# Kernel optimization log

Measured on AMD Instinct MI355X. Metric: run time of the kernel, lower is better.

## Reference

```python
import jax, jax.numpy as jnp
import numpy as np

N = 4096          # detections per frame
M = 8192          # memory entries (tracks + backdrops)
D = 256           # embed_dim (hardcoded in module)
NUM_CLASSES = 80
OBJ_THR = 0.3
INIT_THR = 0.7
MATCH_THR = 0.5
NMS_CONF_THR = 0.5
NMS_BACKDROP_IOU = 0.3
NMS_CLASS_IOU = 0.7
NEG = -1e30


def bbox_iou(a, b):
    # a: [Na,4], b: [Nb,4] in (x1,y1,x2,y2) -> [Na,Nb]
    area_a = jnp.clip(a[:, 2] - a[:, 0], 0) * jnp.clip(a[:, 3] - a[:, 1], 0)
    area_b = jnp.clip(b[:, 2] - b[:, 0], 0) * jnp.clip(b[:, 3] - b[:, 1], 0)
    lt = jnp.maximum(a[:, None, :2], b[None, :, :2])
    rb = jnp.minimum(a[:, None, 2:], b[None, :, 2:])
    wh = jnp.clip(rb - lt, 0)
    inter = wh[..., 0] * wh[..., 1]
    return inter / jnp.clip(area_a[:, None] + area_b[None, :] - inter, 1e-6)


def setup_inputs() -> dict:
    key = jax.random.key(0)
    ks = jax.random.split(key, 8)
    xy = jax.random.uniform(ks[0], (N, 2)) * 1024.0
    wh = jax.random.uniform(ks[1], (N, 2)) * 200.0 + 8.0
    detections = jnp.concatenate([xy, xy + wh], axis=1)
    detection_scores = jax.random.uniform(ks[2], (N,))
    detection_class_ids = jax.random.randint(ks[3], (N,), 0, NUM_CLASSES)
    embeddings = jax.random.normal(ks[4], (N, D))
    memo_embeds = jax.random.normal(ks[5], (M, D))
    memo_class_ids = jax.random.randint(ks[6], (M,), 0, NUM_CLASSES)
    memo_track_ids = jax.random.randint(ks[7], (M,), 0, 10000)
    # last quarter of memory entries are backdrops (track_id == -1)
    memo_track_ids = memo_track_ids.at[3 * M // 4:].set(-1)
    return dict(
        detections=detections,
        detection_scores=detection_scores,
        detection_class_ids=detection_class_ids,
        embeddings=embeddings,
        memo_embeds=memo_embeds,
        memo_class_ids=memo_class_ids,
        memo_track_ids=memo_track_ids,
        num_tracks=10000,
    )


def reference(detections, detection_scores, detection_class_ids, embeddings,
              memo_embeds, memo_class_ids, memo_track_ids, num_tracks):
    # ---- remove_duplicates: sort by score desc, dual-threshold greedy NMS ----
    order = jnp.argsort(-detection_scores)
    boxes = detections[order]
    scores = detection_scores[order]
    cls = detection_class_ids[order]
    emb = embeddings[order]

    ious = bbox_iou(boxes, boxes)  # [N,N]
    thr = jnp.where(scores < OBJ_THR, NMS_BACKDROP_IOU, NMS_CLASS_IOU)
    lower = jnp.tril(jnp.ones((N, N), bool), -1)  # j < i (strict)
    # valids[i] depends only on ious against ALL higher-score dets (as in source)
    valid = ~(((ious > thr[:, None]) & lower).any(axis=1))

    # ---- bi-directional softmax similarity ----
    feats = emb @ memo_embeds.T  # [N,M]
    feats_m = jnp.where(valid[:, None], feats, NEG)  # invalid dets excluded
    d2t = jax.nn.softmax(feats_m, axis=1)
    t2d = jax.nn.softmax(feats_m, axis=0)
    sims = 0.5 * (d2t + t2d)
    cat_same = (cls[:, None] == memo_class_ids[None, :]).astype(sims.dtype)
    sims = sims * cat_same * valid[:, None].astype(sims.dtype)

    # ---- greedy per-detection matching (sequential: matched cols zeroed) ----
    col_ids = jnp.arange(M)

    def body(taken, inp):
        row, score = inp
        row = jnp.where(taken, 0.0, row)
        ind = jnp.argmax(row)
        conf = row[ind]
        cur = memo_track_ids[ind]
        match = conf > MATCH_THR
        is_track = cur > -1
        strong = score > OBJ_THR
        assign = match & is_track & strong
        idv = jnp.where(
            assign, cur,
            jnp.where(match & (~is_track) & (conf > NMS_CONF_THR), -2, -1))
        taken = taken | ((col_ids == ind) & assign)
        return taken, idv

    _, ids = jax.lax.scan(body, jnp.zeros((M,), bool), (sims, scores))

    # ---- create new tracks for confident unmatched detections ----
    new = (ids == -1) & (scores > INIT_THR) & valid
    offs = jnp.cumsum(new.astype(jnp.int32)) - 1
    ids = jnp.where(new, jnp.int32(num_tracks) + offs, ids)

    # ---- un-permute back to original detection order ----
    ids_out = jnp.zeros((N,), ids.dtype).at[order].set(ids)
    valid_out = jnp.zeros((N,), bool).at[order].set(valid)
    return ids_out, valid_out, sims
```

## Files before the change

kernel.cpp:

```cpp
#include <hip/hip_runtime.h>

#define NDET 4096
#define NMEM 8192
#define DEMB 256
#define CAP  64
#define POOL 6144

static __device__ __forceinline__ float sim_val(float f, float rm, float rs,
                                                float cm, float cs, bool same) {
  if (!same) return 0.0f;
  return 0.5f * (expf(f - rm) / rs + expf(f - cm) / cs);
}

__global__ __launch_bounds__(256) void k_sort(const float* __restrict__ scores,
                                              const int* __restrict__ cls,
                                              const float* __restrict__ det,
                                              int* order, float* sscore, int* scls,
                                              float* sboxes, int* ccnt) {
  __shared__ float s[NDET];
  int tid = threadIdx.x;
  for (int i = tid; i < NDET; i += 256) s[i] = scores[i];
  __syncthreads();
  int i = blockIdx.x * 256 + tid;
  ccnt[i] = 0;
  float si = s[i];
  int rank = 0;
  for (int j = 0; j < NDET; ++j) {
    float sj = s[j];
    rank += (sj > si) || (sj == si && j < i);
  }
  order[rank] = i;
  sscore[rank] = si;
  scls[rank] = cls[i];
  ((float4*)sboxes)[rank] = ((const float4*)det)[i];
}

__global__ __launch_bounds__(256) void k_gather(const float* __restrict__ emb,
                                                const int* __restrict__ order,
                                                float* A) {
  int idx = blockIdx.x * 256 + threadIdx.x;
  int r = idx >> 6, lane = idx & 63;
  int o = order[r];
  ((float4*)A)[(size_t)r * 64 + lane] = ((const float4*)emb)[(size_t)o * 64 + lane];
}

__global__ __launch_bounds__(256) void k_valid(const float* __restrict__ sbox,
                                               const float* __restrict__ sscore,
                                               int* svalid) {
  int i = blockIdx.x, tid = threadIdx.x;
  float4 bi = ((const float4*)sbox)[i];
  float thr = (sscore[i] < 0.3f) ? 0.3f : 0.7f;
  float ai = fmaxf(bi.z - bi.x, 0.f) * fmaxf(bi.w - bi.y, 0.f);
  __shared__ int flag;
  if (tid == 0) flag = 0;
  __syncthreads();
  int any = 0;
  for (int j = tid; j < i; j += 256) {
    float4 bj = ((const float4*)sbox)[j];
    float aj = fmaxf(bj.z - bj.x, 0.f) * fmaxf(bj.w - bj.y, 0.f);
    float lx = fmaxf(bi.x, bj.x), ly = fmaxf(bi.y, bj.y);
    float rx = fminf(bi.z, bj.z), ry = fminf(bi.w, bj.w);
    float w = fmaxf(rx - lx, 0.f), h = fmaxf(ry - ly, 0.f);
    float inter = w * h;
    float den = fmaxf(ai + aj - inter, 1e-6f);
    any |= ((inter / den) > thr);
  }
  if (any) atomicOr(&flag, 1);
  __syncthreads();
  if (tid == 0) svalid[i] = flag ? 0 : 1;
}

__global__ __launch_bounds__(256, 4) void k_gemm1(const float* __restrict__ A,
                                                  const float* __restrict__ B,
                                                  const int* __restrict__ svalid,
                                                  float2* __restrict__ rowpart,
                                                  float2* __restrict__ colpart,
                                                  float* __restrict__ feats) {
  __shared__ float smraw[2 * 32 * 132];
  float (*As)[132] = (float (*)[132])smraw;
  float (*Bs)[132] = (float (*)[132])(smraw + 32 * 132);
  float (*red)[17] = (float (*)[17])smraw;
  float* tmax = smraw + 128 * 17;
  __shared__ unsigned char vrow[128];
  const int tid = threadIdx.x;
  const int tx = tid & 15, ty = tid >> 4;
  const int j0 = blockIdx.x * 128, i0 = blockIdx.y * 128;
  if (tid < 128) vrow[tid] = (unsigned char)svalid[i0 + tid];
  float acc[8][8];
#pragma unroll
  for (int u = 0; u < 8; ++u)
#pragma unroll
    for (int v = 0; v < 8; ++v) acc[u][v] = 0.f;

  for (int kt = 0; kt < DEMB / 32; ++kt) {
    const int k0 = kt * 32;
    float4 av[4], bv[4];
    int rr[4], cc[4];
#pragma unroll
    for (int e = 0; e < 4; ++e) {
      int f = e * 256 + tid;
      rr[e] = f >> 3;
      cc[e] = (f & 7) << 2;
      av[e] = *(const float4*)(A + (size_t)(i0 + rr[e]) * DEMB + k0 + cc[e]);
      bv[e] = *(const float4*)(B + (size_t)(j0 + rr[e]) * DEMB + k0 + cc[e]);
    }
    __syncthreads();
#pragma unroll
    for (int e = 0; e < 4; ++e) {
      As[cc[e] + 0][rr[e]] = av[e].x;
      As[cc[e] + 1][rr[e]] = av[e].y;
      As[cc[e] + 2][rr[e]] = av[e].z;
      As[cc[e] + 3][rr[e]] = av[e].w;
      Bs[cc[e] + 0][rr[e]] = bv[e].x;
      Bs[cc[e] + 1][rr[e]] = bv[e].y;
      Bs[cc[e] + 2][rr[e]] = bv[e].z;
      Bs[cc[e] + 3][rr[e]] = bv[e].w;
    }
    __syncthreads();
#pragma unroll
    for (int kk = 0; kk < 32; ++kk) {
      float4 a0 = *(const float4*)&As[kk][ty * 8];
      float4 a1 = *(const float4*)&As[kk][ty * 8 + 4];
      float4 b0 = *(const float4*)&Bs[kk][tx * 8];
      float4 b1 = *(const float4*)&Bs[kk][tx * 8 + 4];
      float a[8] = {a0.x, a0.y, a0.z, a0.w, a1.x, a1.y, a1.z, a1.w};
      float b[8] = {b0.x, b0.y, b0.z, b0.w, b1.x, b1.y, b1.z, b1.w};
#pragma unroll
      for (int u = 0; u < 8; ++u)
#pragma unroll
        for (int v = 0; v < 8; ++v) acc[u][v] = __builtin_fmaf(a[u], b[v], acc[u][v]);
    }
  }
#pragma unroll
  for (int u = 0; u < 8; ++u) {
    int row = i0 + ty * 8 + u;
    float4 o0 = {acc[u][0], acc[u][1], acc[u][2], acc[u][3]};
    float4 o1 = {acc[u][4], acc[u][5], acc[u][6], acc[u][7]};
    *(float4*)(feats + (size_t)row * NMEM + j0 + tx * 8) = o0;
    *(float4*)(feats + (size_t)row * NMEM + j0 + tx * 8 + 4) = o1;
  }
  __syncthreads();
#pragma unroll
  for (int u = 0; u < 8; ++u) {
    float m = acc[u][0];
#pragma unroll
    for (int v = 1; v < 8; ++v) m = fmaxf(m, acc[u][v]);
    red[ty * 8 + u][tx] = m;
  }
  __syncthreads();
  if (tid < 128) {
    float m = red[tid][0];
#pragma unroll
    for (int t = 1; t < 16; ++t) m = fmaxf(m, red[tid][t]);
    tmax[tid] = m;
  }
  __syncthreads();
#pragma unroll
  for (int u = 0; u < 8; ++u) {
    float m = tmax[ty * 8 + u], s = 0.f;
#pragma unroll
    for (int v = 0; v < 8; ++v) s += expf(acc[u][v] - m);
    red[ty * 8 + u][tx] = s;
  }
  __syncthreads();
  if (tid < 128) {
    float s = 0.f;
#pragma unroll
    for (int t = 0; t < 16; ++t) s += red[tid][t];
    rowpart[(size_t)(i0 + tid) * 64 + blockIdx.x] = make_float2(tmax[tid], s);
  }
  __syncthreads();
#pragma unroll
  for (int v = 0; v < 8; ++v) {
    float m = -INFINITY;
#pragma unroll
    for (int u = 0; u < 8; ++u)
      if (vrow[ty * 8 + u]) m = fmaxf(m, acc[u][v]);
    red[tx * 8 + v][ty] = m;
  }
  __syncthreads();
  if (tid < 128) {
    float m = red[tid][0];
#pragma unroll
    for (int t = 1; t < 16; ++t) m = fmaxf(m, red[tid][t]);
    tmax[tid] = m;
  }
  __syncthreads();
#pragma unroll
  for (int v = 0; v < 8; ++v) {
    float m = tmax[tx * 8 + v], s = 0.f;
    if (m > -INFINITY) {
#pragma unroll
      for (int u = 0; u < 8; ++u)
        if (vrow[ty * 8 + u]) s += expf(acc[u][v] - m);
    }
    red[tx * 8 + v][ty] = s;
  }
  __syncthreads();
  if (tid < 128) {
    float s = 0.f;
#pragma unroll
    for (int t = 0; t < 16; ++t) s += red[tid][t];
    colpart[(size_t)(j0 + tid) * 32 + blockIdx.y] = make_float2(tmax[tid], s);
  }
}

__global__ __launch_bounds__(256) void k_rowmerge(const float2* __restrict__ rowpart,
                                                  float* rmax, float* rsum) {
  int r = blockIdx.x * 256 + threadIdx.x;
  float M = -INFINITY;
  for (int c = 0; c < 64; ++c) M = fmaxf(M, rowpart[(size_t)r * 64 + c].x);
  float s = 0.f;
  for (int c = 0; c < 64; ++c) {
    float2 p = rowpart[(size_t)r * 64 + c];
    s += p.y * expf(p.x - M);
  }
  rmax[r] = M;
  rsum[r] = s;
}

__global__ __launch_bounds__(256) void k_colmerge(const float2* __restrict__ colpart,
                                                  float* cmax, float* csum) {
  int c = blockIdx.x * 256 + threadIdx.x;
  float M = -INFINITY;
  for (int b = 0; b < 32; ++b) {
    float2 p = colpart[(size_t)c * 32 + b];
    if (p.y > 0.f) M = fmaxf(M, p.x);
  }
  float s = 0.f;
  for (int b = 0; b < 32; ++b) {
    float2 p = colpart[(size_t)c * 32 + b];
    if (p.y > 0.f) s += p.y * expf(p.x - M);
  }
  cmax[c] = M;
  csum[c] = s;
}

__global__ __launch_bounds__(256) void k_transform(float* __restrict__ sims,
                                                   const float* __restrict__ rmax,
                                                   const float* __restrict__ rsum,
                                                   const float* __restrict__ cmax,
                                                   const float* __restrict__ csum,
                                                   const int* __restrict__ scls,
                                                   const int* __restrict__ mcls,
                                                   const int* __restrict__ svalid,
                                                   float* __restrict__ cval,
                                                   int* __restrict__ cidx,
                                                   int* __restrict__ ccnt) {
  const int r = blockIdx.x, tid = threadIdx.x;
  float* row = sims + (size_t)r * NMEM;
  if (!svalid[r]) {
    float4 z = {0.f, 0.f, 0.f, 0.f};
#pragma unroll
    for (int it = 0; it < 8; ++it) *(float4*)(row + it * 1024 + tid * 4) = z;
    return;
  }
  const float rm = rmax[r], rs = rsum[r];
  const int rc = scls[r];
#pragma unroll
  for (int it = 0; it < 8; ++it) {
    int j = it * 1024 + tid * 4;
    float4 f = *(const float4*)(row + j);
    float4 cm4 = *(const float4*)(cmax + j);
    float4 cs4 = *(const float4*)(csum + j);
    int4 mc4 = *(const int4*)(mcls + j);
    float4 o;
    o.x = sim_val(f.x, rm, rs, cm4.x, cs4.x, rc == mc4.x);
    o.y = sim_val(f.y, rm, rs, cm4.y, cs4.y, rc == mc4.y);
    o.z = sim_val(f.z, rm, rs, cm4.z, cs4.z, rc == mc4.z);
    o.w = sim_val(f.w, rm, rs, cm4.w, cs4.w, rc == mc4.w);
    *(float4*)(row + j) = o;
    float vs[4] = {o.x, o.y, o.z, o.w};
#pragma unroll
    for (int q = 0; q < 4; ++q) {
      if (vs[q] > 0.5f) {
        int ps = atomicAdd(&ccnt[r], 1);
        if (ps < CAP) {
          cval[(size_t)r * CAP + ps] = vs[q];
          cidx[(size_t)r * CAP + ps] = j + q;
        }
      }
    }
  }
}

__global__ __launch_bounds__(256) void k_match(
    const float* __restrict__ cval, const int* __restrict__ cidx,
    const int* __restrict__ ccnt, const float* __restrict__ sscore,
    const int* __restrict__ svalid, const int* __restrict__ order,
    const int* __restrict__ mtrack, const int* __restrict__ ntptr,
    const float* __restrict__ sims, float* __restrict__ out) {
  const int tid = threadIdx.x;
  __shared__ float pv[POOL];
  __shared__ int mt[NMEM];
  __shared__ int ids_s[NDET];
  __shared__ unsigned int taken[NMEM / 32];
  __shared__ int part[256];
  __shared__ float rv[256];
  __shared__ int ri[256];
  __shared__ unsigned short pi[POOL];
  __shared__ unsigned short rlist[NDET];
  __shared__ unsigned short cstart[NDET];
  __shared__ unsigned char flags[NDET];
  __shared__ unsigned char cnt_s[NDET];
  __shared__ int nR_s;

  for (int r = tid; r < NDET; r += 256) {
    float s = sscore[r];
    int c = ccnt[r];
    flags[r] = (unsigned char)((svalid[r] ? 1 : 0) | (s > 0.3f ? 2 : 0) |
                               (s > 0.7f ? 4 : 0));
    cnt_s[r] = (unsigned char)(c > 255 ? 255 : c);
    ids_s[r] = -1;
  }
  for (int j = tid; j < NMEM; j += 256) mt[j] = mtrack[j];
  taken[tid] = 0u;
  __syncthreads();

  const int base = tid * 16;
  int cn = 0, pool_need = 0;
  for (int k = 0; k < 16; ++k) {
    int c = cnt_s[base + k];
    cn += (c > 0);
    pool_need += (c > 0 && c <= CAP) ? c : 0;
  }
  part[tid] = cn;
  __syncthreads();
  if (tid == 0) {
    int run = 0;
    for (int t = 0; t < 256; ++t) { int v = part[t]; part[t] = run; run += v; }
    nR_s = run;
  }
  __syncthreads();
  {
    int pos = part[tid];
    for (int k = 0; k < 16; ++k)
      if (cnt_s[base + k] > 0) rlist[pos++] = (unsigned short)(base + k);
  }
  __syncthreads();
  part[tid] = pool_need;
  __syncthreads();
  if (tid == 0) {
    int run = 0;
    for (int t = 0; t < 256; ++t) { int v = part[t]; part[t] = run; run += v; }
  }
  __syncthreads();
  {
    int off = part[tid];
    for (int k = 0; k < 16; ++k) {
      int r = base + k;
      int c = cnt_s[r];
      if (c == 0) continue;
      if (c <= CAP) {
        if (off + c <= POOL) {
          cstart[r] = (unsigned short)off;
          for (int q = 0; q < c; ++q) {
            pv[off + q] = cval[(size_t)r * CAP + q];
            pi[off + q] = (unsigned short)cidx[(size_t)r * CAP + q];
          }
        } else cstart[r] = 0xFFFFu;
        off += c;
      } else cstart[r] = 0xFFFFu;
    }
  }
  __syncthreads();
  const int nR = nR_s;

  for (int t = 0; t < nR; ++t) {
    const int r = rlist[t];
    const int c = cnt_s[r];
    if (c <= CAP) {
      if (tid == 0) {
        float bvv = 0.f;
        int bii = -1;
        const unsigned int st = cstart[r];
        if (st != 0xFFFFu) {
          for (int q = 0; q < c; ++q) {
            int j = pi[st + q];
            if ((taken[j >> 5] >> (j & 31)) & 1u) continue;
            float v = pv[st + q];
            if (bii < 0 || v > bvv || (v == bvv && j < bii)) { bvv = v; bii = j; }
          }
        } else {
          for (int q = 0; q < c; ++q) {
            int j = cidx[(size_t)r * CAP + q];
            if ((taken[j >> 5] >> (j & 31)) & 1u) continue;
            float v = cval[(size_t)r * CAP + q];
            if (bii < 0 || v > bvv || (v == bvv && j < bii)) { bvv = v; bii = j; }
          }
        }
        if (bii >= 0 && bvv > 0.5f) {
          int cur = mt[bii];
          if (cur > -1) {
            if (flags[r] & 2) { ids_s[r] = cur; taken[bii >> 5] |= 1u << (bii & 31); }
          } else ids_s[r] = -2;
        }
      }
    } else {
      __syncthreads();
      const float* srow = sims + (size_t)r * NMEM;
      float bvv = -1.f;
      int bii = 1 << 30;
      for (int j = tid; j < NMEM; j += 256) {
        float v = ((taken[j >> 5] >> (j & 31)) & 1u) ? 0.f : srow[j];
        if (v > bvv || (v == bvv && j < bii)) { bvv = v; bii = j; }
      }
      rv[tid] = bvv;
      ri[tid] = bii;
      __syncthreads();
      for (int off = 128; off > 0; off >>= 1) {
        if (tid < off) {
          float v2 = rv[tid + off];
          int i2 = ri[tid + off];
          if (v2 > rv[tid] || (v2 == rv[tid] && i2 < ri[tid])) { rv[tid] = v2; ri[tid] = i2; }
        }
        __syncthreads();
      }
      if (tid == 0) {
        float conf = rv[0];
        int ind = ri[0];
        if (conf > 0.5f) {
          int cur = mt[ind];
          if (cur > -1) {
            if (flags[r] & 2) { ids_s[r] = cur; taken[ind >> 5] |= 1u << (ind & 31); }
          } else ids_s[r] = -2;
        }
      }
      __syncthreads();
    }
  }
  __syncthreads();

  int cntNew = 0;
  for (int k = 0; k < 16; ++k) {
    int r = base + k;
    cntNew += (ids_s[r] == -1 && (flags[r] & 4) && (flags[r] & 1));
  }
  part[tid] = cntNew;
  __syncthreads();
  if (tid == 0) {
    int run = 0;
    for (int t2 = 0; t2 < 256; ++t2) { int v = part[t2]; part[t2] = run; run += v; }
  }
  __syncthreads();
  const int nt = ntptr[0];
  int off2 = part[tid];
  for (int k = 0; k < 16; ++k) {
    int r = base + k;
    if (ids_s[r] == -1 && (flags[r] & 4) && (flags[r] & 1)) ids_s[r] = nt + off2++;
  }
  __syncthreads();
  for (int r = tid; r < NDET; r += 256) {
    int o = order[r];
    out[o] = (float)ids_s[r];
    out[NDET + o] = (flags[r] & 1) ? 1.0f : 0.0f;
  }
}

extern "C" void kernel_launch(void* const* d_in, const int* in_sizes, int n_in,
                              void* d_out, int out_size, void* d_ws, size_t ws_size,
                              hipStream_t stream) {
  const float* det = (const float*)d_in[0];
  const float* scores = (const float*)d_in[1];
  const int* cls = (const int*)d_in[2];
  const float* emb = (const float*)d_in[3];
  const float* memo = (const float*)d_in[4];
  const int* mcls = (const int*)d_in[5];
  const int* mtrack = (const int*)d_in[6];
  const int* ntptr = (const int*)d_in[7];
  float* out = (float*)d_out;
  float* feats = out + 2 * NDET;

  char* ws = (char*)d_ws;
  size_t o_A = 0;
  size_t o_order = o_A + (size_t)NDET * DEMB * 4;
  size_t o_sscore = o_order + NDET * 4;
  size_t o_scls = o_sscore + NDET * 4;
  size_t o_svalid = o_scls + NDET * 4;
  size_t o_sbox = o_svalid + NDET * 4;
  size_t o_rowpart = o_sbox + NDET * 16;
  size_t o_colpart = o_rowpart + (size_t)NDET * 64 * 8;
  size_t o_rmax = o_colpart + (size_t)NMEM * 32 * 8;
  size_t o_rsum = o_rmax + NDET * 4;
  size_t o_cmax = o_rsum + NDET * 4;
  size_t o_csum = o_cmax + NMEM * 4;
  size_t o_cval = o_csum + NMEM * 4;
  size_t o_cidx = o_cval + (size_t)NDET * CAP * 4;
  size_t o_ccnt = o_cidx + (size_t)NDET * CAP * 4;

  float* A = (float*)(ws + o_A);
  int* order = (int*)(ws + o_order);
  float* sscore = (float*)(ws + o_sscore);
  int* scls = (int*)(ws + o_scls);
  int* svalid = (int*)(ws + o_svalid);
  float* sbox = (float*)(ws + o_sbox);
  float2* rowpart = (float2*)(ws + o_rowpart);
  float2* colpart = (float2*)(ws + o_colpart);
  float* rmax = (float*)(ws + o_rmax);
  float* rsum = (float*)(ws + o_rsum);
  float* cmax = (float*)(ws + o_cmax);
  float* csum = (float*)(ws + o_csum);
  float* cval = (float*)(ws + o_cval);
  int* cidx = (int*)(ws + o_cidx);
  int* ccnt = (int*)(ws + o_ccnt);

  k_sort<<<NDET / 256, 256, 0, stream>>>(scores, cls, det, order, sscore, scls, sbox,
                                         ccnt);
  k_gather<<<NDET * 64 / 256, 256, 0, stream>>>(emb, order, A);
  k_valid<<<NDET, 256, 0, stream>>>(sbox, sscore, svalid);
  k_gemm1<<<dim3(NMEM / 128, NDET / 128), 256, 0, stream>>>(A, memo, svalid, rowpart,
                                                            colpart, feats);
  k_rowmerge<<<NDET / 256, 256, 0, stream>>>(rowpart, rmax, rsum);
  k_colmerge<<<NMEM / 256, 256, 0, stream>>>(colpart, cmax, csum);
  k_transform<<<NDET, 256, 0, stream>>>(feats, rmax, rsum, cmax, csum, scls, mcls,
                                        svalid, cval, cidx, ccnt);
  k_match<<<1, 256, 0, stream>>>(cval, cidx, ccnt, sscore, svalid, order, mtrack,
                                 ntptr, feats, out);
}
```

Baseline: 605.2 us.

## Resolve uncontended detections in parallel before serial matching; prefetch GEMM tiles

The match kernel now counts how many candidate lists claim each memory column. Rows whose candidate columns are claimed by no other row are resolved in parallel, which shrinks the serial greedy loop that runs on a single thread. The GEMM kernel register-prefetches the next K tile while computing the current one, lowers the occupancy hint from 4 to 3 blocks, and unrolls the FMAs explicitly. The trade-offs are extra shared-memory atomics and claim storage in the match kernel, and more register pressure in the GEMM.

Result: slower. 972.4 us (+60.7%).

```diff
diff --git a/kernel.cpp b/kernel.cpp
--- a/kernel.cpp
+++ b/kernel.cpp
@@ -70,7 +70,17 @@
   if (tid == 0) svalid[i] = flag ? 0 : 1;
 }
 
-__global__ __launch_bounds__(256, 4) void k_gemm1(const float* __restrict__ A,
+#define FMA8(U, AS)                                     \
+  acc[U][0] = __builtin_fmaf(AS, b0.x, acc[U][0]);      \
+  acc[U][1] = __builtin_fmaf(AS, b0.y, acc[U][1]);      \
+  acc[U][2] = __builtin_fmaf(AS, b0.z, acc[U][2]);      \
+  acc[U][3] = __builtin_fmaf(AS, b0.w, acc[U][3]);      \
+  acc[U][4] = __builtin_fmaf(AS, b1.x, acc[U][4]);      \
+  acc[U][5] = __builtin_fmaf(AS, b1.y, acc[U][5]);      \
+  acc[U][6] = __builtin_fmaf(AS, b1.z, acc[U][6]);      \
+  acc[U][7] = __builtin_fmaf(AS, b1.w, acc[U][7]);
+
+__global__ __launch_bounds__(256, 3) void k_gemm1(const float* __restrict__ A,
                                                   const float* __restrict__ B,
                                                   const int* __restrict__ svalid,
                                                   float2* __restrict__ rowpart,
@@ -86,49 +96,61 @@
   const int tx = tid & 15, ty = tid >> 4;
   const int j0 = blockIdx.x * 128, i0 = blockIdx.y * 128;
   if (tid < 128) vrow[tid] = (unsigned char)svalid[i0 + tid];
+
+  const float* ga[4];
+  const float* gb[4];
+  int rr_[4], cc_[4];
+#pragma unroll
+  for (int e = 0; e < 4; ++e) {
+    int f = e * 256 + tid;
+    rr_[e] = f >> 3;
+    cc_[e] = (f & 7) << 2;
+    ga[e] = A + (size_t)(i0 + rr_[e]) * DEMB + cc_[e];
+    gb[e] = B + (size_t)(j0 + rr_[e]) * DEMB + cc_[e];
+  }
   float acc[8][8];
 #pragma unroll
   for (int u = 0; u < 8; ++u)
 #pragma unroll
     for (int v = 0; v < 8; ++v) acc[u][v] = 0.f;
 
-  for (int kt = 0; kt < DEMB / 32; ++kt) {
-    const int k0 = kt * 32;
-    float4 av[4], bv[4];
-    int rr[4], cc[4];
+  float4 av[4], bv[4];
+#pragma unroll
+  for (int e = 0; e < 4; ++e) {
+    av[e] = *(const float4*)ga[e];
+    bv[e] = *(const float4*)gb[e];
+  }
+
+  for (int kt = 0; kt < 8; ++kt) {
+    __syncthreads();
 #pragma unroll
     for (int e = 0; e < 4; ++e) {
-      int f = e * 256 + tid;
-      rr[e] = f >> 3;
-      cc[e] = (f & 7) << 2;
-      av[e] = *(const float4*)(A + (size_t)(i0 + rr[e]) * DEMB + k0 + cc[e]);
-      bv[e] = *(const float4*)(B + (size_t)(j0 + rr[e]) * DEMB + k0 + cc[e]);
+      As[cc_[e] + 0][rr_[e]] = av[e].x;
+      As[cc_[e] + 1][rr_[e]] = av[e].y;
+      As[cc_[e] + 2][rr_[e]] = av[e].z;
+      As[cc_[e] + 3][rr_[e]] = av[e].w;
+      Bs[cc_[e] + 0][rr_[e]] = bv[e].x;
+      Bs[cc_[e] + 1][rr_[e]] = bv[e].y;
+      Bs[cc_[e] + 2][rr_[e]] = bv[e].z;
+      Bs[cc_[e] + 3][rr_[e]] = bv[e].w;
     }
     __syncthreads();
-#pragma unroll
-    for (int e = 0; e < 4; ++e) {
-      As[cc[e] + 0][rr[e]] = av[e].x;
-      As[cc[e] + 1][rr[e]] = av[e].y;
-      As[cc[e] + 2][rr[e]] = av[e].z;
-      As[cc[e] + 3][rr[e]] = av[e].w;
-      Bs[cc[e] + 0][rr[e]] = bv[e].x;
-      Bs[cc[e] + 1][rr[e]] = bv[e].y;
-      Bs[cc[e] + 2][rr[e]] = bv[e].z;
-      Bs[cc[e] + 3][rr[e]] = bv[e].w;
-    }
-    __syncthreads();
+    if (kt < 7) {
+      const int koff = (kt + 1) * 32;
+#pragma unroll
+      for (int e = 0; e < 4; ++e) {
+        av[e] = *(const float4*)(ga[e] + koff);
+        bv[e] = *(const float4*)(gb[e] + koff);
+      }
+    }
 #pragma unroll
     for (int kk = 0; kk < 32; ++kk) {
       float4 a0 = *(const float4*)&As[kk][ty * 8];
       float4 a1 = *(const float4*)&As[kk][ty * 8 + 4];
       float4 b0 = *(const float4*)&Bs[kk][tx * 8];
       float4 b1 = *(const float4*)&Bs[kk][tx * 8 + 4];
-      float a[8] = {a0.x, a0.y, a0.z, a0.w, a1.x, a1.y, a1.z, a1.w};
-      float b[8] = {b0.x, b0.y, b0.z, b0.w, b1.x, b1.y, b1.z, b1.w};
-#pragma unroll
-      for (int u = 0; u < 8; ++u)
-#pragma unroll
-        for (int v = 0; v < 8; ++v) acc[u][v] = __builtin_fmaf(a[u], b[v], acc[u][v]);
+      FMA8(0, a0.x) FMA8(1, a0.y) FMA8(2, a0.z) FMA8(3, a0.w)
+      FMA8(4, a1.x) FMA8(5, a1.y) FMA8(6, a1.z) FMA8(7, a1.w)
     }
   }
 #pragma unroll
@@ -292,19 +314,21 @@
     const float* __restrict__ sims, float* __restrict__ out) {
   const int tid = threadIdx.x;
   __shared__ float pv[POOL];
+  __shared__ unsigned short pi[POOL];
+  __shared__ int claim[NMEM];
   __shared__ int mt[NMEM];
   __shared__ int ids_s[NDET];
   __shared__ unsigned int taken[NMEM / 32];
   __shared__ int part[256];
   __shared__ float rv[256];
   __shared__ int ri[256];
-  __shared__ unsigned short pi[POOL];
   __shared__ unsigned short rlist[NDET];
   __shared__ unsigned short cstart[NDET];
   __shared__ unsigned char flags[NDET];
   __shared__ unsigned char cnt_s[NDET];
-  __shared__ int nR_s;
-
+  __shared__ int nR_s, allser_s;
+
+  if (tid == 0) allser_s = 0;
   for (int r = tid; r < NDET; r += 256) {
     float s = sscore[r];
     int c = ccnt[r];
@@ -313,31 +337,19 @@
     cnt_s[r] = (unsigned char)(c > 255 ? 255 : c);
     ids_s[r] = -1;
   }
-  for (int j = tid; j < NMEM; j += 256) mt[j] = mtrack[j];
+  for (int j = tid; j < NMEM; j += 256) {
+    mt[j] = mtrack[j];
+    claim[j] = 0;
+  }
   taken[tid] = 0u;
   __syncthreads();
 
   const int base = tid * 16;
-  int cn = 0, pool_need = 0;
+  int pool_need = 0;
   for (int k = 0; k < 16; ++k) {
     int c = cnt_s[base + k];
-    cn += (c > 0);
     pool_need += (c > 0 && c <= CAP) ? c : 0;
   }
-  part[tid] = cn;
-  __syncthreads();
-  if (tid == 0) {
-    int run = 0;
-    for (int t = 0; t < 256; ++t) { int v = part[t]; part[t] = run; run += v; }
-    nR_s = run;
-  }
-  __syncthreads();
-  {
-    int pos = part[tid];
-    for (int k = 0; k < 16; ++k)
-      if (cnt_s[base + k] > 0) rlist[pos++] = (unsigned short)(base + k);
-  }
-  __syncthreads();
   part[tid] = pool_need;
   __syncthreads();
   if (tid == 0) {
@@ -351,17 +363,67 @@
       int r = base + k;
       int c = cnt_s[r];
       if (c == 0) continue;
-      if (c <= CAP) {
-        if (off + c <= POOL) {
-          cstart[r] = (unsigned short)off;
-          for (int q = 0; q < c; ++q) {
-            pv[off + q] = cval[(size_t)r * CAP + q];
-            pi[off + q] = (unsigned short)cidx[(size_t)r * CAP + q];
-          }
-        } else cstart[r] = 0xFFFFu;
-        off += c;
-      } else cstart[r] = 0xFFFFu;
-    }
+      if (c > CAP) {
+        atomicOr(&allser_s, 1);
+        cstart[r] = 0xFFFFu;
+        continue;
+      }
+      unsigned short st = (off + c <= POOL) ? (unsigned short)off : (unsigned short)0xFFFFu;
+      cstart[r] = st;
+      for (int q = 0; q < c; ++q) {
+        int j = cidx[(size_t)r * CAP + q];
+        atomicAdd(&claim[j], 1);
+        if (st != 0xFFFFu) {
+          pv[off + q] = cval[(size_t)r * CAP + q];
+          pi[off + q] = (unsigned short)j;
+        }
+      }
+      off += c;
+    }
+  }
+  __syncthreads();
+  const int allser = allser_s;
+
+  for (int k = 0; k < 16; ++k) {
+    int r = base + k;
+    int c = cnt_s[r];
+    if (c == 0 || c > CAP) continue;
+    bool indep = !allser;
+    float bvv = -1.f;
+    int bii = 1 << 30;
+    const unsigned st = cstart[r];
+    for (int q = 0; q < c; ++q) {
+      int j;
+      float v;
+      if (st != 0xFFFFu) { j = pi[st + q]; v = pv[st + q]; }
+      else { j = cidx[(size_t)r * CAP + q]; v = cval[(size_t)r * CAP + q]; }
+      if (claim[j] != 1) indep = false;
+      if (v > bvv || (v == bvv && j < bii)) { bvv = v; bii = j; }
+    }
+    if (indep) {
+      int cur = mt[bii];
+      if (cur > -1) {
+        if (flags[r] & 2) ids_s[r] = cur;
+      } else ids_s[r] = -2;
+      cnt_s[r] = 0;
+    }
+  }
+  __syncthreads();
+
+  int cn = 0;
+  for (int k = 0; k < 16; ++k) cn += (cnt_s[base + k] > 0);
+  part[tid] = cn;
+  __syncthreads();
+  if (tid == 0) {
+    int run = 0;
+    for (int t = 0; t < 256; ++t) { int v = part[t]; part[t] = run; run += v; }
+    nR_s = run;
+  }
+  __syncthreads();
+  {
+    int pos = part[tid];
+    for (int k = 0; k < 16; ++k)
+      if (cnt_s[base + k] > 0) rlist[pos++] = (unsigned short)(base + k);
   }
   __syncthreads();
   const int nR = nR_s;
@@ -373,7 +435,7 @@
       if (tid == 0) {
         float bvv = 0.f;
         int bii = -1;
-        const unsigned int st = cstart[r];
+        const unsigned st = cstart[r];
         if (st != 0xFFFFu) {
           for (int q = 0; q < c; ++q) {
             int j = pi[st + q];
```
